# Optimization experiments

Hardware: AMD Instinct MI355X
Metric: run time of the kernel (lower is better)

The kernel has to match this reference:

```python
import jax, jax.numpy as jnp
import numpy as np

H = 1024      # hidden_size
NH = 16       # num_attention_heads
HD = H // NH  # attention_head_size = 64
FF = 4096     # intermediate_size
EPS = 1e-5


def setup_inputs() -> dict:
    key = jax.random.key(0)
    ks = jax.random.split(key, 16)
    B, S = 8, 512
    s = lambda d: 1.0 / np.sqrt(d)
    return {
        "hidden_states": jax.random.normal(ks[0], (B, S, H), jnp.float32),
        "attention_mask": jnp.zeros((B, 1, 1, S), jnp.float32),  # additive mask
        "wq": jax.random.normal(ks[1], (H, H), jnp.float32) * s(H),
        "bq": jnp.zeros((H,), jnp.float32),
        "wk": jax.random.normal(ks[2], (H, H), jnp.float32) * s(H),
        "bk": jnp.zeros((H,), jnp.float32),
        "wv": jax.random.normal(ks[3], (H, H), jnp.float32) * s(H),
        "bv": jnp.zeros((H,), jnp.float32),
        "wo": jax.random.normal(ks[4], (H, H), jnp.float32) * s(H),
        "bo": jnp.zeros((H,), jnp.float32),
        "ln1_g": jnp.ones((H,), jnp.float32),
        "ln1_b": jnp.zeros((H,), jnp.float32),
        "wi": jax.random.normal(ks[5], (H, FF), jnp.float32) * s(H),
        "bi": jnp.zeros((FF,), jnp.float32),
        "wo2": jax.random.normal(ks[6], (FF, H), jnp.float32) * s(FF),
        "bo2": jnp.zeros((H,), jnp.float32),
        "ln2_g": jnp.ones((H,), jnp.float32),
        "ln2_b": jnp.zeros((H,), jnp.float32),
    }


def _layer_norm(x, g, b):
    mu = jnp.mean(x, axis=-1, keepdims=True)
    var = jnp.mean(jnp.square(x - mu), axis=-1, keepdims=True)
    return (x - mu) * jax.lax.rsqrt(var + EPS) * g + b


def reference(hidden_states, attention_mask, wq, bq, wk, bk, wv, bv,
              wo, bo, ln1_g, ln1_b, wi, bi, wo2, bo2, ln2_g, ln2_b):
    B, S, _ = hidden_states.shape
    split = lambda x: x.reshape(B, S, NH, HD).transpose(0, 2, 1, 3)  # [B,NH,S,HD]
    q = split(hidden_states @ wq + bq)
    k = split(hidden_states @ wk + bk)
    v = split(hidden_states @ wv + bv)
    # scaled dot-product attention with additive mask (dropout = eval identity)
    scores = jnp.einsum("bhqd,bhkd->bhqk", q, k) / np.sqrt(HD)
    scores = scores + attention_mask
    probs = jax.nn.softmax(scores, axis=-1)
    ctx = jnp.einsum("bhqk,bhkd->bhqd", probs, v)
    ctx = ctx.transpose(0, 2, 1, 3).reshape(B, S, H)
    # RobertaSelfOutput: dense + residual + LayerNorm
    attn_out = _layer_norm(ctx @ wo + bo + hidden_states, ln1_g, ln1_b)
    # FFN: intermediate (gelu) + output dense + residual + LayerNorm
    inter = jax.nn.gelu(attn_out @ wi + bi, approximate=False)
    layer_out = _layer_norm(inter @ wo2 + bo2 + attn_out, ln2_g, ln2_b)
    return layer_out
```

## Files before the change

kernel.cpp:

```cpp
#include <hip/hip_runtime.h>
#include <math.h>

#define DI __device__ __forceinline__

typedef unsigned short u16;
typedef __attribute__((ext_vector_type(8))) u16 u16x8;
typedef __attribute__((ext_vector_type(4))) u16 u16x4;
typedef __attribute__((ext_vector_type(8))) __bf16 bf16x8;
typedef __attribute__((ext_vector_type(4))) float f32x4;

typedef const __attribute__((address_space(1))) unsigned int g_u32;
typedef __attribute__((address_space(3))) unsigned int l_u32;

DI float bf2f(u16 u) {
  unsigned v = ((unsigned)u) << 16;
  float f; __builtin_memcpy(&f, &v, 4); return f;
}
DI u16 f2bf(float f) {
  unsigned u; __builtin_memcpy(&u, &f, 4);
  u += 0x7fff + ((u >> 16) & 1);
  return (u16)(u >> 16);
}
DI f32x4 mfma16(bf16x8 a, bf16x8 b, f32x4 c) {
  return __builtin_amdgcn_mfma_f32_16x16x32_bf16(a, b, c, 0, 0, 0);
}
DI void gl16(const void* g, const u16* lds) {
  __builtin_amdgcn_global_load_lds((g_u32*)g, (l_u32*)lds, 16, 0, 0);
}

__global__ __launch_bounds__(256) void cvt_bf16_k(const float* __restrict__ in,
                                                  u16* __restrict__ out, int n) {
  int i = (blockIdx.x * 256 + threadIdx.x) * 8;
  if (i >= n) return;
  float4 a = *(const float4*)(in + i);
  float4 b = *(const float4*)(in + i + 4);
  u16x8 o;
  o[0] = f2bf(a.x); o[1] = f2bf(a.y); o[2] = f2bf(a.z); o[3] = f2bf(a.w);
  o[4] = f2bf(b.x); o[5] = f2bf(b.y); o[6] = f2bf(b.z); o[7] = f2bf(b.w);
  *(u16x8*)(out + i) = o;
}

__global__ __launch_bounds__(256) void tcvt_k(const float* __restrict__ in,
                                              u16* __restrict__ out, int K, int N) {
  __shared__ float tile[32][33];
  int n0 = blockIdx.x * 32, k0 = blockIdx.y * 32;
  int tx = threadIdx.x & 31, ty = threadIdx.x >> 5;
  #pragma unroll
  for (int i = 0; i < 4; i++) {
    int kr = ty + i * 8;
    tile[kr][tx] = in[(size_t)(k0 + kr) * N + n0 + tx];
  }
  __syncthreads();
  #pragma unroll
  for (int i = 0; i < 4; i++) {
    int nr = ty + i * 8;
    out[(size_t)(n0 + nr) * K + k0 + tx] = f2bf(tile[tx][nr]);
  }
}

__global__ __launch_bounds__(256) void pack_bias_k(const float* __restrict__ b0,
                                                   const float* __restrict__ b1,
                                                   const float* __restrict__ b2,
                                                   float* __restrict__ out) {
  int i = blockIdx.x * 256 + threadIdx.x;
  float v = (i < 1024) ? b0[i] : (i < 2048 ? b1[i - 1024] : b2[i - 2048]);
  out[i] = v;
}

#define QUAD(d, mh, nh) do {                                                          \
  const u16* Ab_ = &sA[d][wr][0];                                                     \
  const u16* Bb_ = &sB[d][wc >> 1][0];                                                \
  bf16x8 af_[4][2], bv_[2][2];                                                        \
  _Pragma("unroll") for (int i_ = 0; i_ < 4; i_++) {                                  \
    int row_ = (mh) * 64 + i_ * 16 + r15;                                             \
    _Pragma("unroll") for (int ks_ = 0; ks_ < 2; ks_++)                               \
      af_[i_][ks_] = *(const bf16x8*)&Ab_[row_ * 64 + ((((ks_ << 2) | kg) + row_) & 7) * 8]; } \
  _Pragma("unroll") for (int j_ = 0; j_ < 2; j_++) {                                  \
    int row_ = (wc & 1) * 64 + (nh) * 32 + j_ * 16 + r15;                             \
    _Pragma("unroll") for (int ks_ = 0; ks_ < 2; ks_++)                               \
      bv_[j_][ks_] = *(const bf16x8*)&Bb_[row_ * 64 + ((((ks_ << 2) | kg) + row_) & 7) * 8]; } \
  __builtin_amdgcn_s_barrier();                                                       \
  __builtin_amdgcn_s_setprio(1);                                                      \
  _Pragma("unroll") for (int i_ = 0; i_ < 4; i_++)                                    \
    _Pragma("unroll") for (int j_ = 0; j_ < 2; j_++)                                  \
      _Pragma("unroll") for (int ks_ = 0; ks_ < 2; ks_++)                             \
        acc[(mh) * 4 + i_][(nh) * 2 + j_] =                                           \
            mfma16(af_[i_][ks_], bv_[j_][ks_], acc[(mh) * 4 + i_][(nh) * 2 + j_]);    \
  __builtin_amdgcn_s_setprio(0);                                                      \
} while (0)

template<int EPI, int SPLITK>
__global__ __launch_bounds__(512, 2) void gemm8p_k(const u16* __restrict__ A,
                                                   const u16* __restrict__ Bt,
                                                   const float* __restrict__ bias,
                                                   void* __restrict__ out,
                                                   int M, int N, int K) {
  __shared__ __align__(16) u16 sA[2][2][128 * 64];
  __shared__ __align__(16) u16 sB[2][2][128 * 64];
  const int tid = threadIdx.x;
  const int lane = tid & 63, wid = tid >> 6;
  const int wr = wid >> 2, wc = wid & 3;
  const int r15 = lane & 15, kg = lane >> 4;

  const int GX = gridDim.x, GY = gridDim.y;
  int nwg = GX * GY;
  int orig = blockIdx.y * GX + blockIdx.x;
  int s = (orig & 7) * (nwg >> 3) + (orig >> 3);
  int bx = s / GY, by = s - bx * GY;
  const int bm = by * 256, bn = bx * 256;

  const int z = blockIdx.z;
  int tilesK = K >> 6;
  int qs = tilesK / SPLITK, rs = tilesK - qs * SPLITK;
  int ntz = qs + (z < rs ? 1 : 0);
  int k0 = (z * qs + (z < rs ? z : rs)) << 6;

  f32x4 acc[8][4];
  #pragma unroll
  for (int i = 0; i < 8; i++)
    #pragma unroll
    for (int j = 0; j < 4; j++) acc[i][j] = (f32x4){0.f, 0.f, 0.f, 0.f};

  const int drw = tid >> 3;
  const int gsl8 = ((tid - drw) & 7) << 3;
  const u16* pA0 = A  + (size_t)(bm +       drw) * K + k0 + gsl8;
  const u16* pA1 = A  + (size_t)(bm + 128 + drw) * K + k0 + gsl8;
  const u16* pB0 = Bt + (size_t)(bn +       drw) * K + k0 + gsl8;
  const u16* pB1 = Bt + (size_t)(bn + 128 + drw) * K + k0 + gsl8;
  const size_t s2o = (size_t)64 * K;
  const int dld = wid << 9;

  auto stageTile = [&](int d) {
    u16* dA0 = &sA[d][0][dld]; u16* dA1 = &sA[d][1][dld];
    u16* dB0 = &sB[d][0][dld]; u16* dB1 = &sB[d][1][dld];
    gl16(pA0, dA0); gl16(pA0 + s2o, dA0 + 4096);
    gl16(pB0, dB0); gl16(pB0 + s2o, dB0 + 4096);
    gl16(pA1, dA1); gl16(pA1 + s2o, dA1 + 4096);
    gl16(pB1, dB1); gl16(pB1 + s2o, dB1 + 4096);
    pA0 += 64; pA1 += 64; pB0 += 64; pB1 += 64;
  };

  stageTile(0);
  if (ntz > 1) stageTile(1);

  for (int t = 0; t < ntz; ++t) {
    int d = t & 1;
    if (t + 1 < ntz) asm volatile("s_waitcnt vmcnt(8)" ::: "memory");
    else             asm volatile("s_waitcnt vmcnt(0)" ::: "memory");
    __builtin_amdgcn_s_barrier();
    QUAD(d, 0, 0);
    QUAD(d, 0, 1);
    QUAD(d, 1, 0);
    QUAD(d, 1, 1);
    __builtin_amdgcn_s_barrier();
    __builtin_amdgcn_sched_barrier(0);
    if (t + 2 < ntz) stageTile(d);
  }

  #pragma unroll
  for (int ii = 0; ii < 8; ii++) {
    int row = bm + wr * 128 + ii * 16 + kg * 4;
    #pragma unroll
    for (int jj = 0; jj < 4; jj++) {
      int col = bn + wc * 64 + jj * 16 + r15;
      if (EPI == 4) {
        size_t zoff = (size_t)z * M * N;
        #pragma unroll
        for (int q2 = 0; q2 < 4; q2++)
          ((float*)out)[zoff + (size_t)(row + q2) * N + col] = acc[ii][jj][q2];
      } else {
        float bv = bias[col];
        #pragma unroll
        for (int q2 = 0; q2 < 4; q2++) {
          float v = acc[ii][jj][q2] + bv;
          if (EPI == 2) v = 0.5f * v * (1.0f + erff(v * 0.70710678118f));
          ((u16*)out)[(size_t)(row + q2) * N + col] = f2bf(v);
        }
      }
    }
  }
}

template<int EPI>
__global__ __launch_bounds__(256) void gemm_bt_k(const u16* __restrict__ A,
                                                 const u16* __restrict__ Bt,
                                                 const float* __restrict__ bias,
                                                 const void* __restrict__ resid,
                                                 u16* __restrict__ out,
                                                 int M, int N, int K) {
  __shared__ __align__(16) u16 As[2][128 * 64];
  __shared__ __align__(16) u16 Bs[2][128 * 64];
  const int tid = threadIdx.x;
  const int lane = tid & 63, wid = tid >> 6;
  const int wm = (wid >> 1) * 64, wn = (wid & 1) * 64;
  const int r15 = lane & 15, kg = lane >> 4;
  const int srow = lane >> 3;

  const int GX = gridDim.x, GY = gridDim.y;
  int nwg = GX * GY;
  int orig = blockIdx.y * GX + blockIdx.x;
  int s = (orig & 7) * (nwg >> 3) + (orig >> 3);
  int bx = s / GY, by = s - bx * GY;
  const int bm = by * 128, bn = bx * 128;

  f32x4 acc[4][4];
  #pragma unroll
  for (int i = 0; i < 4; i++)
    #pragma unroll
    for (int j = 0; j < 4; j++) acc[i][j] = (f32x4){0.f, 0.f, 0.f, 0.f};

  const u16* pAc[4]; const u16* pBc[4];
  #pragma unroll
  for (int c = 0; c < 4; c++) {
    int chunk = (c << 2) | wid;
    int row = (chunk << 3) + srow;
    int gsl = ((lane & 7) - row) & 7;
    pAc[c] = A  + (size_t)(bm + row) * K + (gsl << 3);
    pBc[c] = Bt + (size_t)(bn + row) * K + (gsl << 3);
  }
  auto STAGE = [&](int buf, int kt) {
    #pragma unroll
    for (int c = 0; c < 4; c++) {
      int chunk = (c << 2) | wid;
      gl16(pAc[c] + kt, &As[buf][chunk << 9]);
      gl16(pBc[c] + kt, &Bs[buf][chunk << 9]);
    }
  };
  auto COMPUTE = [&](int buf) {
    #pragma unroll
    for (int ks = 0; ks < 2; ks++) {
      bf16x8 af[4], bfr[4];
      #pragma unroll
      for (int i = 0; i < 4; i++) {
        int row = wm + i * 16 + r15;
        af[i] = *(const bf16x8*)&As[buf][row * 64 + (((ks << 2) + kg + row) & 7) * 8];
      }
      #pragma unroll
      for (int i = 0; i < 4; i++) {
        int row = wn + i * 16 + r15;
        bfr[i] = *(const bf16x8*)&Bs[buf][row * 64 + (((ks << 2) + kg + row) & 7) * 8];
      }
      #pragma unroll
      for (int i = 0; i < 4; i++)
        #pragma unroll
        for (int j = 0; j < 4; j++)
          acc[i][j] = mfma16(af[i], bfr[j], acc[i][j]);
    }
  };

  const int nt = K >> 6;
  STAGE(0, 0);
  if (nt > 1) STAGE(1, 64);
  for (int t = 0; t < nt; ++t) {
    if (t + 1 < nt) asm volatile("s_waitcnt vmcnt(8)" ::: "memory");
    else            asm volatile("s_waitcnt vmcnt(0)" ::: "memory");
    __builtin_amdgcn_s_barrier();
    COMPUTE(t & 1);
    __builtin_amdgcn_s_barrier();
    __builtin_amdgcn_sched_barrier(0);
    if (t + 2 < nt) STAGE(t & 1, (t + 2) << 6);
  }

  #pragma unroll
  for (int i = 0; i < 4; i++) {
    int row0 = bm + wm + i * 16 + kg * 4;
    #pragma unroll
    for (int j = 0; j < 4; j++) {
      int col = bn + wn + j * 16 + r15;
      float bv = bias[col];
      #pragma unroll
      for (int q2 = 0; q2 < 4; q2++) {
        int row = row0 + q2;
        float v = acc[i][j][q2] + bv;
        if (EPI == 1) v += ((const float*)resid)[(size_t)row * N + col];
        out[(size_t)row * N + col] = f2bf(v);
      }
    }
  }
}

__global__ __launch_bounds__(256) void attn_k(const u16* __restrict__ QKV,
                                              const float* __restrict__ mask,
                                              u16* __restrict__ ctx) {
  __shared__ __align__(16) u16 sQ[32 * 72];
  __shared__ __align__(16) u16 sK[64 * 72];
  __shared__ __align__(16) u16 sVt[64 * 72];
  __shared__ __align__(16) u16 sS[32 * 520];
  __shared__ float sSum[32];
  const int t = threadIdx.x, lane = t & 63, wid = t >> 6;
  const int qb = blockIdx.x, h = blockIdx.y, b = blockIdx.z;
  const int r15 = lane & 15, kg = lane >> 4;
  const int mg = wid >> 1, half = wid & 1;
  const size_t qoff = (size_t)h * 64;
  const size_t koff = 1024 + qoff, voff = 2048 + qoff;

  {
    int row = t >> 3, d0 = (t & 7) * 8;
    *(u16x8*)&sQ[row * 72 + d0] =
        *(const u16x8*)&QKV[((size_t)(b * 512 + qb * 32 + row)) * 3072 + qoff + d0];
  }

  for (int kt = 0; kt < 8; ++kt) {
    int row = t >> 2, d0 = (t & 3) * 16;
    const u16* src = &QKV[((size_t)(b * 512 + kt * 64 + row)) * 3072 + koff + d0];
    *(u16x8*)&sK[row * 72 + d0] = *(const u16x8*)src;
    *(u16x8*)&sK[row * 72 + d0 + 8] = *(const u16x8*)(src + 8);
    __syncthreads();
    bf16x8 qf0 = *(const bf16x8*)&sQ[(mg * 16 + r15) * 72 + kg * 8];
    bf16x8 qf1 = *(const bf16x8*)&sQ[(mg * 16 + r15) * 72 + 32 + kg * 8];
    #pragma unroll
    for (int n2 = 0; n2 < 2; n2++) {
      int nt = half * 2 + n2;
      f32x4 sacc = (f32x4){0.f, 0.f, 0.f, 0.f};
      sacc = mfma16(qf0, *(const bf16x8*)&sK[(nt * 16 + r15) * 72 + kg * 8], sacc);
      sacc = mfma16(qf1, *(const bf16x8*)&sK[(nt * 16 + r15) * 72 + 32 + kg * 8], sacc);
      int col = kt * 64 + nt * 16 + r15;
      float mv = mask[b * 512 + col];
      #pragma unroll
      for (int q = 0; q < 4; q++) {
        int rl = mg * 16 + kg * 4 + q;
        sS[rl * 520 + col] = f2bf(sacc[q] * 0.125f + mv);
      }
    }
    __syncthreads();
  }

  {
    int row = t >> 3, seg = t & 7;
    float mx = -1e30f;
    for (int j = 0; j < 64; j++)
      mx = fmaxf(mx, bf2f(sS[row * 520 + seg * 64 + j]));
    mx = fmaxf(mx, __shfl_xor(mx, 1));
    mx = fmaxf(mx, __shfl_xor(mx, 2));
    mx = fmaxf(mx, __shfl_xor(mx, 4));
    float sum = 0.f;
    for (int j = 0; j < 64; j++) {
      int idx = row * 520 + seg * 64 + j;
      float p = __expf(bf2f(sS[idx]) - mx);
      sum += p;
      sS[idx] = f2bf(p);
    }
    sum += __shfl_xor(sum, 1);
    sum += __shfl_xor(sum, 2);
    sum += __shfl_xor(sum, 4);
    if (seg == 0) sSum[row] = sum;
  }
  __syncthreads();

  f32x4 pacc[2];
  pacc[0] = (f32x4){0.f, 0.f, 0.f, 0.f};
  pacc[1] = (f32x4){0.f, 0.f, 0.f, 0.f};
  for (int vt = 0; vt < 8; ++vt) {
    int rowk = t >> 2, d0 = (t & 3) * 16;
    const u16* src = &QKV[((size_t)(b * 512 + vt * 64 + rowk)) * 3072 + voff + d0];
    u16x8 v0 = *(const u16x8*)src;
    u16x8 v1 = *(const u16x8*)(src + 8);
    #pragma unroll
    for (int e = 0; e < 8; e++) {
      sVt[(d0 + e) * 72 + rowk] = v0[e];
      sVt[(d0 + 8 + e) * 72 + rowk] = v1[e];
    }
    __syncthreads();
    bf16x8 pf0 = *(const bf16x8*)&sS[(mg * 16 + r15) * 520 + vt * 64 + kg * 8];
    bf16x8 pf1 = *(const bf16x8*)&sS[(mg * 16 + r15) * 520 + vt * 64 + 32 + kg * 8];
    #pragma unroll
    for (int n2 = 0; n2 < 2; n2++) {
      int dcol = half * 32 + n2 * 16;
      pacc[n2] = mfma16(pf0, *(const bf16x8*)&sVt[(dcol + r15) * 72 + kg * 8], pacc[n2]);
      pacc[n2] = mfma16(pf1, *(const bf16x8*)&sVt[(dcol + r15) * 72 + 32 + kg * 8], pacc[n2]);
    }
    __syncthreads();
  }
  #pragma unroll
  for (int n2 = 0; n2 < 2; n2++) {
    int d = half * 32 + n2 * 16 + r15;
    #pragma unroll
    for (int q = 0; q < 4; q++) {
      int rl = mg * 16 + kg * 4 + q;
      float v = pacc[n2][q] / sSum[rl];
      ctx[((size_t)(b * 512 + qb * 32 + rl)) * 1024 + qoff + d] = f2bf(v);
    }
  }
}

template<int OUTF32>
__global__ __launch_bounds__(256) void ln_k(const u16* __restrict__ in,
                                            const float* __restrict__ g,
                                            const float* __restrict__ be,
                                            void* __restrict__ out) {
  int row = blockIdx.x, t = threadIdx.x;
  const u16* rp = in + (size_t)row * 1024 + t * 4;
  u16x4 raw = *(const u16x4*)rp;
  float x[4];
  #pragma unroll
  for (int i = 0; i < 4; i++) x[i] = bf2f(raw[i]);
  float s = x[0] + x[1] + x[2] + x[3];
  float q = x[0]*x[0] + x[1]*x[1] + x[2]*x[2] + x[3]*x[3];
  #pragma unroll
  for (int off = 32; off; off >>= 1) {
    s += __shfl_down(s, off);
    q += __shfl_down(q, off);
  }
  __shared__ float rs_[4], rq_[4];
  int wid = t >> 6, lane = t & 63;
  if (!lane) { rs_[wid] = s; rq_[wid] = q; }
  __syncthreads();
  float S1 = rs_[0] + rs_[1] + rs_[2] + rs_[3];
  float S2 = rq_[0] + rq_[1] + rq_[2] + rq_[3];
  float mu = S1 * (1.0f / 1024.0f);
  float inv = rsqrtf(S2 * (1.0f / 1024.0f) - mu * mu + 1e-5f);
  #pragma unroll
  for (int i = 0; i < 4; i++) {
    int c = t * 4 + i;
    float y = (x[i] - mu) * inv * g[c] + be[c];
    if (OUTF32) ((float*)out)[(size_t)row * 1024 + c] = y;
    else        ((u16*)out)[(size_t)row * 1024 + c] = f2bf(y);
  }
}

__global__ __launch_bounds__(256) void ln2r_k(const float* __restrict__ part,
                                              const float* __restrict__ bias,
                                              const u16* __restrict__ resid,
                                              const float* __restrict__ g,
                                              const float* __restrict__ be,
                                              float* __restrict__ out) {
  const int row = blockIdx.x, t = threadIdx.x;
  const size_t base = (size_t)row * 1024 + t * 4;
  float4 p0 = *(const float4*)(part + base);
  float4 p1 = *(const float4*)(part + 4194304 + base);
  float4 p2 = *(const float4*)(part + 8388608 + base);
  u16x4 rr = *(const u16x4*)(resid + base);
  float x[4];
  x[0] = p0.x + p1.x + p2.x + bias[t*4+0] + bf2f(rr[0]);
  x[1] = p0.y + p1.y + p2.y + bias[t*4+1] + bf2f(rr[1]);
  x[2] = p0.z + p1.z + p2.z + bias[t*4+2] + bf2f(rr[2]);
  x[3] = p0.w + p1.w + p2.w + bias[t*4+3] + bf2f(rr[3]);
  float s = x[0] + x[1] + x[2] + x[3];
  float q = x[0]*x[0] + x[1]*x[1] + x[2]*x[2] + x[3]*x[3];
  #pragma unroll
  for (int off = 32; off; off >>= 1) {
    s += __shfl_down(s, off);
    q += __shfl_down(q, off);
  }
  __shared__ float rs_[4], rq_[4];
  int wid = t >> 6, lane = t & 63;
  if (!lane) { rs_[wid] = s; rq_[wid] = q; }
  __syncthreads();
  float S1 = rs_[0] + rs_[1] + rs_[2] + rs_[3];
  float S2 = rq_[0] + rq_[1] + rq_[2] + rq_[3];
  float mu = S1 * (1.0f / 1024.0f);
  float inv = rsqrtf(S2 * (1.0f / 1024.0f) - mu * mu + 1e-5f);
  #pragma unroll
  for (int i = 0; i < 4; i++) {
    int c = t * 4 + i;
    out[(size_t)row * 1024 + c] = (x[i] - mu) * inv * g[c] + be[c];
  }
}

extern "C" void kernel_launch(void* const* d_in, const int* in_sizes, int n_in,
                              void* d_out, int out_size, void* d_ws, size_t ws_size,
                              hipStream_t stream) {
  const float* hidden = (const float*)d_in[0];
  const float* mask   = (const float*)d_in[1];
  const float* wq  = (const float*)d_in[2];  const float* bq  = (const float*)d_in[3];
  const float* wk  = (const float*)d_in[4];  const float* bk  = (const float*)d_in[5];
  const float* wv  = (const float*)d_in[6];  const float* bv  = (const float*)d_in[7];
  const float* wo  = (const float*)d_in[8];  const float* bo  = (const float*)d_in[9];
  const float* ln1g = (const float*)d_in[10]; const float* ln1b = (const float*)d_in[11];
  const float* wi  = (const float*)d_in[12]; const float* bi  = (const float*)d_in[13];
  const float* wo2 = (const float*)d_in[14]; const float* bo2 = (const float*)d_in[15];
  const float* ln2g = (const float*)d_in[16]; const float* ln2b = (const float*)d_in[17];

  char* ws = (char*)d_ws;
  u16*   WqkvT = (u16*)(ws + 0);
  u16*   WoT   = (u16*)(ws + 6291456);
  u16*   Xb    = (u16*)(ws + 8388608);
  u16*   QKVb  = (u16*)(ws + 16777216);
  u16*   Ctx   = (u16*)(ws + 41943040);
  u16*   AD    = (u16*)(ws + 50331648);
  float* part  = (float*)(ws + 0);
  u16*   AO    = (u16*)(ws + 58720256);
  u16*   Inter = (u16*)(ws + 67108864);
  u16*   WiT   = (u16*)(ws + 100663296);
  u16*   Wo2T  = (u16*)(ws + 109051904);
  float* bqkv  = (float*)(ws + 117440512);

  cvt_bf16_k<<<2048, 256, 0, stream>>>(hidden, Xb, 4194304);
  tcvt_k<<<dim3(32, 32),  256, 0, stream>>>(wq,  WqkvT,                1024, 1024);
  tcvt_k<<<dim3(32, 32),  256, 0, stream>>>(wk,  WqkvT + 1024 * 1024,  1024, 1024);
  tcvt_k<<<dim3(32, 32),  256, 0, stream>>>(wv,  WqkvT + 2048 * 1024,  1024, 1024);
  tcvt_k<<<dim3(32, 32),  256, 0, stream>>>(wo,  WoT,  1024, 1024);
  tcvt_k<<<dim3(128, 32), 256, 0, stream>>>(wi,  WiT,  1024, 4096);
  tcvt_k<<<dim3(32, 128), 256, 0, stream>>>(wo2, Wo2T, 4096, 1024);
  pack_bias_k<<<12, 256, 0, stream>>>(bq, bk, bv, bqkv);

  gemm8p_k<0, 1><<<dim3(12, 16, 1), 512, 0, stream>>>(Xb, WqkvT, bqkv, QKVb, 4096, 3072, 1024);

  attn_k<<<dim3(16, 16, 8), 256, 0, stream>>>(QKVb, mask, Ctx);

  gemm_bt_k<1><<<dim3(8, 32), 256, 0, stream>>>(Ctx, WoT, bo, hidden, AD, 4096, 1024, 1024);
  ln_k<0><<<4096, 256, 0, stream>>>(AD, ln1g, ln1b, AO);

  gemm8p_k<2, 1><<<dim3(16, 16, 1), 512, 0, stream>>>(AO, WiT, bi, Inter, 4096, 4096, 1024);

  gemm8p_k<4, 3><<<dim3(4, 16, 3), 512, 0, stream>>>(Inter, Wo2T, nullptr, part, 4096, 1024, 4096);

  ln2r_k<<<4096, 256, 0, stream>>>(part, bo2, AO, ln2g, ln2b, (float*)d_out);
}
```

Baseline: 412.0 us.

## Replace materialized-score attention with flash-style online-softmax kernel and pre-transposed V

The attention kernel no longer writes the full 32x512 score tile to LDS and runs a separate softmax pass. It now computes online softmax in registers over 64-key tiles, with each wave handling 32 query rows. A separate kernel transposes V into a per-head layout. K and V tiles are double-buffered through direct global-to-LDS loads with swizzled addressing, and P is rearranged across lanes with ds_bpermute to feed the PV MFMA. The goal is fewer LDS round trips and barriers and fewer blocks reloading K/V; the costs are an extra launch, an extra pass over V, and higher register pressure.

```diff
diff --git a/kernel.cpp b/kernel.cpp
--- a/kernel.cpp
+++ b/kernel.cpp
@@ -26,6 +26,11 @@
 }
 DI void gl16(const void* g, const u16* lds) {
   __builtin_amdgcn_global_load_lds((g_u32*)g, (l_u32*)lds, 16, 0, 0);
+}
+DI unsigned cvtpk(float lo, float hi) {
+  unsigned d;
+  asm("v_cvt_pk_bf16_f32 %0, %1, %2" : "=v"(d) : "v"(lo), "v"(hi));
+  return d;
 }
 
 __global__ __launch_bounds__(256) void cvt_bf16_k(const float* __restrict__ in,
@@ -65,6 +70,28 @@
   int i = blockIdx.x * 256 + threadIdx.x;
   float v = (i < 1024) ? b0[i] : (i < 2048 ? b1[i - 1024] : b2[i - 2048]);
   out[i] = v;
+}
+
+__global__ __launch_bounds__(256) void vtr_k(const u16* __restrict__ QKV,
+                                             u16* __restrict__ VT) {
+  __shared__ u16 tile[64][72];
+  const int t = threadIdx.x;
+  const int kt = blockIdx.x, bh = blockIdx.y;
+  const int b = bh >> 4, h = bh & 15;
+  {
+    int r = t >> 2, d0 = (t & 3) * 16;
+    const u16* src = &QKV[((size_t)(b * 512 + kt * 64 + r)) * 3072 + 2048 + h * 64 + d0];
+    *(u16x8*)&tile[r][d0] = *(const u16x8*)src;
+    *(u16x8*)&tile[r][d0 + 8] = *(const u16x8*)(src + 8);
+  }
+  __syncthreads();
+  int d = t >> 2, kseg = (t & 3) * 16;
+  u16x8 o0, o1;
+  #pragma unroll
+  for (int j = 0; j < 8; j++) { o0[j] = tile[kseg + j][d]; o1[j] = tile[kseg + 8 + j][d]; }
+  u16* dst = &VT[((size_t)bh << 15) + (size_t)d * 512 + kt * 64 + kseg];
+  *(u16x8*)dst = o0;
+  *(u16x8*)(dst + 8) = o1;
 }
 
 #define QUAD(d, mh, nh) do {                                                          \
@@ -279,107 +306,170 @@
   }
 }
 
-__global__ __launch_bounds__(256) void attn_k(const u16* __restrict__ QKV,
-                                              const float* __restrict__ mask,
-                                              u16* __restrict__ ctx) {
-  __shared__ __align__(16) u16 sQ[32 * 72];
-  __shared__ __align__(16) u16 sK[64 * 72];
-  __shared__ __align__(16) u16 sVt[64 * 72];
-  __shared__ __align__(16) u16 sS[32 * 520];
-  __shared__ float sSum[32];
+__global__ __launch_bounds__(256) void fattn_k(const u16* __restrict__ QKV,
+                                               const u16* __restrict__ VT,
+                                               const float* __restrict__ mask,
+                                               u16* __restrict__ ctx) {
+  __shared__ __align__(16) u16 sK[2][64 * 64];
+  __shared__ __align__(16) u16 sV[2][64 * 64];
+  __shared__ float sMask[512];
   const int t = threadIdx.x, lane = t & 63, wid = t >> 6;
+  const int q15 = lane & 15, g = lane >> 4;
   const int qb = blockIdx.x, h = blockIdx.y, b = blockIdx.z;
-  const int r15 = lane & 15, kg = lane >> 4;
-  const int mg = wid >> 1, half = wid & 1;
-  const size_t qoff = (size_t)h * 64;
-  const size_t koff = 1024 + qoff, voff = 2048 + qoff;
-
-  {
-    int row = t >> 3, d0 = (t & 7) * 8;
-    *(u16x8*)&sQ[row * 72 + d0] =
-        *(const u16x8*)&QKV[((size_t)(b * 512 + qb * 32 + row)) * 3072 + qoff + d0];
-  }
+  const int bh = b * 16 + h;
+  const int qrow0 = qb * 128 + wid * 32;
+
+  if (t < 128) *(float4*)&sMask[t * 4] = *(const float4*)&mask[b * 512 + t * 4];
+
+  bf16x8 qf[2][2];
+  #pragma unroll
+  for (int qt = 0; qt < 2; qt++)
+    #pragma unroll
+    for (int c = 0; c < 2; c++)
+      qf[qt][c] = *(const bf16x8*)&QKV[(size_t)(b * 512 + qrow0 + qt * 16 + q15) * 3072 +
+                                       h * 64 + c * 32 + g * 8];
+
+  const int srow0 = t >> 3;
+  const int ssl = (((t & 7) - (t >> 3)) & 7) << 3;
+  const u16* pK = QKV + (size_t)(b * 512 + srow0) * 3072 + 1024 + h * 64 + ssl;
+  const u16* pV = VT + ((size_t)bh << 15) + (size_t)srow0 * 512 + ssl;
+  const size_t kS2 = (size_t)32 * 3072;
+  const size_t vS2 = (size_t)32 * 512;
+  const int dld = t * 8;
+
+  auto stage = [&](int d) {
+    gl16(pK, &sK[d][dld]); gl16(pK + kS2, &sK[d][dld + 2048]);
+    gl16(pV, &sV[d][dld]); gl16(pV + vS2, &sV[d][dld + 2048]);
+    pK += 64 * 3072; pV += 64;
+  };
+
+  stage(0); stage(1);
+
+  float m_[2] = {-1e30f, -1e30f}, l_[2] = {0.f, 0.f};
+  f32x4 oacc[2][4];
+  #pragma unroll
+  for (int qt = 0; qt < 2; qt++)
+    #pragma unroll
+    for (int dt = 0; dt < 4; dt++) oacc[qt][dt] = (f32x4){0.f, 0.f, 0.f, 0.f};
+
+  const int bp0 = ((g & 1) * 32 + q15) * 4;
+  const int bp1 = bp0 + 64;
 
   for (int kt = 0; kt < 8; ++kt) {
-    int row = t >> 2, d0 = (t & 3) * 16;
-    const u16* src = &QKV[((size_t)(b * 512 + kt * 64 + row)) * 3072 + koff + d0];
-    *(u16x8*)&sK[row * 72 + d0] = *(const u16x8*)src;
-    *(u16x8*)&sK[row * 72 + d0 + 8] = *(const u16x8*)(src + 8);
-    __syncthreads();
-    bf16x8 qf0 = *(const bf16x8*)&sQ[(mg * 16 + r15) * 72 + kg * 8];
-    bf16x8 qf1 = *(const bf16x8*)&sQ[(mg * 16 + r15) * 72 + 32 + kg * 8];
-    #pragma unroll
-    for (int n2 = 0; n2 < 2; n2++) {
-      int nt = half * 2 + n2;
-      f32x4 sacc = (f32x4){0.f, 0.f, 0.f, 0.f};
-      sacc = mfma16(qf0, *(const bf16x8*)&sK[(nt * 16 + r15) * 72 + kg * 8], sacc);
-      sacc = mfma16(qf1, *(const bf16x8*)&sK[(nt * 16 + r15) * 72 + 32 + kg * 8], sacc);
-      int col = kt * 64 + nt * 16 + r15;
-      float mv = mask[b * 512 + col];
-      #pragma unroll
-      for (int q = 0; q < 4; q++) {
-        int rl = mg * 16 + kg * 4 + q;
-        sS[rl * 520 + col] = f2bf(sacc[q] * 0.125f + mv);
+    const int d = kt & 1;
+    if (kt < 7) asm volatile("s_waitcnt vmcnt(4)" ::: "memory");
+    else        asm volatile("s_waitcnt vmcnt(0)" ::: "memory");
+    __builtin_amdgcn_s_barrier();
+
+    f32x4 sc[2][4];
+    #pragma unroll
+    for (int qt = 0; qt < 2; qt++)
+      #pragma unroll
+      for (int k16 = 0; k16 < 4; k16++) sc[qt][k16] = (f32x4){0.f, 0.f, 0.f, 0.f};
+    #pragma unroll
+    for (int k16 = 0; k16 < 4; k16++) {
+      int row = k16 * 16 + q15;
+      bf16x8 ak0 = *(const bf16x8*)&sK[d][row * 64 + ((g + row) & 7) * 8];
+      bf16x8 ak1 = *(const bf16x8*)&sK[d][row * 64 + ((4 + g + row) & 7) * 8];
+      #pragma unroll
+      for (int qt = 0; qt < 2; qt++) {
+        sc[qt][k16] = mfma16(ak0, qf[qt][0], sc[qt][k16]);
+        sc[qt][k16] = mfma16(ak1, qf[qt][1], sc[qt][k16]);
       }
     }
-    __syncthreads();
-  }
-
-  {
-    int row = t >> 3, seg = t & 7;
-    float mx = -1e30f;
-    for (int j = 0; j < 64; j++)
-      mx = fmaxf(mx, bf2f(sS[row * 520 + seg * 64 + j]));
-    mx = fmaxf(mx, __shfl_xor(mx, 1));
-    mx = fmaxf(mx, __shfl_xor(mx, 2));
-    mx = fmaxf(mx, __shfl_xor(mx, 4));
-    float sum = 0.f;
-    for (int j = 0; j < 64; j++) {
-      int idx = row * 520 + seg * 64 + j;
-      float p = __expf(bf2f(sS[idx]) - mx);
-      sum += p;
-      sS[idx] = f2bf(p);
+
+    float mk[4][4];
+    #pragma unroll
+    for (int k16 = 0; k16 < 4; k16++)
+      #pragma unroll
+      for (int r = 0; r < 4; r++)
+        mk[k16][r] = sMask[kt * 64 + k16 * 16 + g * 4 + r];
+    float p[2][16];
+    #pragma unroll
+    for (int qt = 0; qt < 2; qt++)
+      #pragma unroll
+      for (int k16 = 0; k16 < 4; k16++)
+        #pragma unroll
+        for (int r = 0; r < 4; r++)
+          p[qt][k16 * 4 + r] = sc[qt][k16][r] * 0.125f + mk[k16][r];
+
+    #pragma unroll
+    for (int qt = 0; qt < 2; qt++) {
+      float tmax = p[qt][0];
+      #pragma unroll
+      for (int j = 1; j < 16; j++) tmax = fmaxf(tmax, p[qt][j]);
+      tmax = fmaxf(tmax, __shfl_xor(tmax, 16));
+      tmax = fmaxf(tmax, __shfl_xor(tmax, 32));
+      float mn = fmaxf(m_[qt], tmax);
+      float al = __expf(m_[qt] - mn);
+      m_[qt] = mn;
+      float ts = 0.f;
+      #pragma unroll
+      for (int j = 0; j < 16; j++) { p[qt][j] = __expf(p[qt][j] - mn); ts += p[qt][j]; }
+      ts += __shfl_xor(ts, 16);
+      ts += __shfl_xor(ts, 32);
+      l_[qt] = l_[qt] * al + ts;
+      #pragma unroll
+      for (int r = 0; r < 4; r++) {
+        float alq = __shfl(al, g * 4 + r);
+        #pragma unroll
+        for (int dt = 0; dt < 4; dt++) oacc[qt][dt][r] *= alq;
+      }
     }
-    sum += __shfl_xor(sum, 1);
-    sum += __shfl_xor(sum, 2);
-    sum += __shfl_xor(sum, 4);
-    if (seg == 0) sSum[row] = sum;
-  }
-  __syncthreads();
-
-  f32x4 pacc[2];
-  pacc[0] = (f32x4){0.f, 0.f, 0.f, 0.f};
-  pacc[1] = (f32x4){0.f, 0.f, 0.f, 0.f};
-  for (int vt = 0; vt < 8; ++vt) {
-    int rowk = t >> 2, d0 = (t & 3) * 16;
-    const u16* src = &QKV[((size_t)(b * 512 + vt * 64 + rowk)) * 3072 + voff + d0];
-    u16x8 v0 = *(const u16x8*)src;
-    u16x8 v1 = *(const u16x8*)(src + 8);
-    #pragma unroll
-    for (int e = 0; e < 8; e++) {
-      sVt[(d0 + e) * 72 + rowk] = v0[e];
-      sVt[(d0 + 8 + e) * 72 + rowk] = v1[e];
+
+    unsigned dwp[2][4][2];
+    #pragma unroll
+    for (int qt = 0; qt < 2; qt++)
+      #pragma unroll
+      for (int k16 = 0; k16 < 4; k16++) {
+        dwp[qt][k16][0] = cvtpk(p[qt][k16 * 4 + 0], p[qt][k16 * 4 + 1]);
+        dwp[qt][k16][1] = cvtpk(p[qt][k16 * 4 + 2], p[qt][k16 * 4 + 3]);
+      }
+
+    #pragma unroll
+    for (int cp = 0; cp < 2; cp++) {
+      bf16x8 pa[2];
+      #pragma unroll
+      for (int qt = 0; qt < 2; qt++) {
+        union { unsigned u[4]; bf16x8 v; } pu;
+        #pragma unroll
+        for (int pp = 0; pp < 2; pp++) {
+          unsigned a0 = __builtin_amdgcn_ds_bpermute(bp0, (int)dwp[qt][2 * cp][pp]);
+          unsigned b0 = __builtin_amdgcn_ds_bpermute(bp0, (int)dwp[qt][2 * cp + 1][pp]);
+          unsigned a1 = __builtin_amdgcn_ds_bpermute(bp1, (int)dwp[qt][2 * cp][pp]);
+          unsigned b1 = __builtin_amdgcn_ds_bpermute(bp1, (int)dwp[qt][2 * cp + 1][pp]);
+          pu.u[pp] = (g & 2) ? b0 : a0;
+          pu.u[2 + pp] = (g & 2) ? b1 : a1;
+        }
+        pa[qt] = pu.v;
+      }
+      #pragma unroll
+      for (int dt = 0; dt < 4; dt++) {
+        int row = dt * 16 + q15;
+        bf16x8 vf = *(const bf16x8*)&sV[d][row * 64 + (((cp << 2) + g + row) & 7) * 8];
+        oacc[0][dt] = mfma16(pa[0], vf, oacc[0][dt]);
+        oacc[1][dt] = mfma16(pa[1], vf, oacc[1][dt]);
+      }
     }
-    __syncthreads();
-    bf16x8 pf0 = *(const bf16x8*)&sS[(mg * 16 + r15) * 520 + vt * 64 + kg * 8];
-    bf16x8 pf1 = *(const bf16x8*)&sS[(mg * 16 + r15) * 520 + vt * 64 + 32 + kg * 8];
-    #pragma unroll
-    for (int n2 = 0; n2 < 2; n2++) {
-      int dcol = half * 32 + n2 * 16;
-      pacc[n2] = mfma16(pf0, *(const bf16x8*)&sVt[(dcol + r15) * 72 + kg * 8], pacc[n2]);
-      pacc[n2] = mfma16(pf1, *(const bf16x8*)&sVt[(dcol + r15) * 72 + 32 + kg * 8], pacc[n2]);
-    }
-    __syncthreads();
-  }
-  #pragma unroll
-  for (int n2 = 0; n2 < 2; n2++) {
-    int d = half * 32 + n2 * 16 + r15;
-    #pragma unroll
-    for (int q = 0; q < 4; q++) {
-      int rl = mg * 16 + kg * 4 + q;
-      float v = pacc[n2][q] / sSum[rl];
-      ctx[((size_t)(b * 512 + qb * 32 + rl)) * 1024 + qoff + d] = f2bf(v);
-    }
+
+    __builtin_amdgcn_s_barrier();
+    __builtin_amdgcn_sched_barrier(0);
+    if (kt + 2 < 8) stage(d);
+  }
+
+  #pragma unroll
+  for (int qt = 0; qt < 2; qt++) {
+    float linv[4];
+    #pragma unroll
+    for (int r = 0; r < 4; r++) linv[r] = 1.0f / __shfl(l_[qt], g * 4 + r);
+    #pragma unroll
+    for (int dt = 0; dt < 4; dt++)
+      #pragma unroll
+      for (int r = 0; r < 4; r++) {
+        int row = qrow0 + qt * 16 + g * 4 + r;
+        ctx[(size_t)(b * 512 + row) * 1024 + h * 64 + dt * 16 + q15] =
+            f2bf(oacc[qt][dt][r] * linv[r]);
+      }
   }
 }
 
@@ -475,6 +565,7 @@
   u16*   WqkvT = (u16*)(ws + 0);
   u16*   WoT   = (u16*)(ws + 6291456);
   u16*   Xb    = (u16*)(ws + 8388608);
+  u16*   VTb   = (u16*)(ws + 8388608);
   u16*   QKVb  = (u16*)(ws + 16777216);
   u16*   Ctx   = (u16*)(ws + 41943040);
   u16*   AD    = (u16*)(ws + 50331648);
@@ -496,7 +587,9 @@
 
   gemm8p_k<0, 1><<<dim3(12, 16, 1), 512, 0, stream>>>(Xb, WqkvT, bqkv, QKVb, 4096, 3072, 1024);
 
-  attn_k<<<dim3(16, 16, 8), 256, 0, stream>>>(QKVb, mask, Ctx);
+  vtr_k<<<dim3(8, 128), 256, 0, stream>>>(QKVb, VTb);
+
+  fattn_k<<<dim3(4, 16, 8), 256, 0, stream>>>(QKVb, VTb, mask, Ctx);
 
   gemm_bt_k<1><<<dim3(8, 32), 256, 0, stream>>>(Ctx, WoT, bo, hidden, AD, 4096, 1024, 1024);
   ln_k<0><<<4096, 256, 0, stream>>>(AD, ln1g, ln1b, AO);
```

Measured after the change: 374.2 us. 9.2% less time.
